# Kernel optimization log

Hardware: AMD Instinct MI355X
Metric: run time of the kernel (lower is better)

Reference implementation:

```python
import jax, jax.numpy as jnp
import numpy as np

EPS = 1e-5  # torch LayerNorm default

def ln(x, g, b):
    mu = jnp.mean(x, axis=-1, keepdims=True)
    var = jnp.mean((x - mu) ** 2, axis=-1, keepdims=True)
    return (x - mu) * jax.lax.rsqrt(var + EPS) * g + b

B, S, E, A = 131072, 199, 3, 32
D_IN = S + 1  # state_dim + 1 (time feature)

def setup_inputs() -> dict:
    key = jax.random.key(0)
    ks = iter(jax.random.split(key, 32))
    def w(shape, fan_in):
        lim = 1.0 / np.sqrt(fan_in)
        return jax.random.uniform(next(ks), shape, jnp.float32, -lim, lim)
    inp = {
        "state": jax.random.normal(next(ks), (B, S), jnp.float32),
        "time_delta": jax.random.uniform(next(ks), (B,), jnp.float32),
        # trunk: Linear(200,256)+LN, Linear(256,256)+LN, Linear(256,128)+LN
        "W1": w((D_IN, 256), D_IN), "b1": w((256,), D_IN),
        "g1": jnp.ones((256,), jnp.float32), "be1": jnp.zeros((256,), jnp.float32),
        "W2": w((256, 256), 256), "b2": w((256,), 256),
        "g2": jnp.ones((256,), jnp.float32), "be2": jnp.zeros((256,), jnp.float32),
        "W3": w((256, 128), 256), "b3": w((128,), 256),
        "g3": jnp.ones((128,), jnp.float32), "be3": jnp.zeros((128,), jnp.float32),
        # value stream
        "Wv1": w((128, 64), 128), "bv1": w((64,), 128),
        "gv": jnp.ones((64,), jnp.float32), "bev": jnp.zeros((64,), jnp.float32),
        "Wv2": w((64, 1), 64), "bv2": w((1,), 64),
        # E stacked advantage streams (all heads share action dim A)
        "Wa1": w((E, 128, 64), 128), "ba1": w((E, 64), 128),
        "ga": jnp.ones((E, 64), jnp.float32), "bea": jnp.zeros((E, 64), jnp.float32),
        "Wa2": w((E, 64, A), 64), "ba2": w((E, A), 64),
        "event_type": jax.random.randint(next(ks), (B,), 0, E),
    }
    return inp

def reference(state, time_delta,
              W1, b1, g1, be1, W2, b2, g2, be2, W3, b3, g3, be3,
              Wv1, bv1, gv, bev, Wv2, bv2,
              Wa1, ba1, ga, bea, Wa2, ba2, event_type):
    td = time_delta[:, None]                       # [B,1]
    x = jnp.concatenate([state, td], axis=1)       # [B,200]
    h = jax.nn.relu(ln(x @ W1 + b1, g1, be1))      # [B,256]
    h = jax.nn.relu(ln(h @ W2 + b2, g2, be2))      # [B,256]
    f = jax.nn.relu(ln(h @ W3 + b3, g3, be3))      # [B,128]
    v = jax.nn.relu(ln(f @ Wv1 + bv1, gv, bev)) @ Wv2 + bv2  # [B,1]
    # compute all E advantage heads, then per-sample select by event_type
    h1 = jnp.einsum('bd,edh->ebh', f, Wa1) + ba1[:, None, :]           # [E,B,64]
    h1 = jax.nn.relu(ln(h1, ga[:, None, :], bea[:, None, :]))
    adv_all = jnp.einsum('ebh,eha->eba', h1, Wa2) + ba2[:, None, :]    # [E,B,A]
    adv = jnp.take_along_axis(adv_all, event_type[None, :, None], axis=0)[0]  # [B,A]
    return v + (adv - adv.mean(axis=1, keepdims=True))
```

## Files before the change

kernel.cpp:

```cpp
#include <hip/hip_runtime.h>
#include <hip/hip_bf16.h>
#include <stdint.h>

#define DEV __device__ __forceinline__

typedef __attribute__((ext_vector_type(8))) short short8;
typedef __attribute__((ext_vector_type(4))) float floatx4;

constexpr int TM  = 64;
constexpr int NB  = 131072;
constexpr int AST = 264;

constexpr int OFF_W1 = 0;
constexpr int OFF_W2 = 57344;
constexpr int OFF_W3 = 122880;
constexpr int OFF_WH = 155648;
constexpr int OFF_WA2= 188416;
constexpr int NWQ    = 194560;

constexpr int C_B1=0, C_G1=256, C_BE1=512, C_B2=768, C_G2=1024, C_BE2=1280,
  C_B3=1536, C_G3=1664, C_BE3=1792, C_BV1=1920, C_GV=1984, C_BEV=2048,
  C_WV2=2112, C_BV2=2176, C_BA1=2180, C_GA=2372, C_BEA=2564, C_BA2=2756;
constexpr int NCONST=2852;

struct Ptrs {
  const float *state,*td,*W1,*b1,*g1,*be1,*W2,*b2,*g2,*be2,*W3,*b3,*g3,*be3,
    *Wv1,*bv1,*gv,*bev,*Wv2,*bv2,*Wa1,*ba1,*ga,*bea,*Wa2,*ba2;
  const int *et;
};

DEV unsigned short f2bf(float x){
  uint32_t u = __float_as_uint(x);
  u += 0x7fffu + ((u>>16)&1u);
  return (unsigned short)(u>>16);
}
DEV uint32_t f2bf_pk(float a, float b){
  float2 f2; f2.x=a; f2.y=b;
  __hip_bfloat162 h = __float22bfloat162_rn(f2);
  union { __hip_bfloat162 h; uint32_t u; } cv; cv.h = h;
  return cv.u;
}

__global__ void prep_kernel(Ptrs p, unsigned short* __restrict__ wq, float* __restrict__ cq){
  int idx = blockIdx.x*256 + threadIdx.x;
  if (idx < NWQ) {
    float v = 0.f;
    if (idx < OFF_W2) {
      int e = idx, w = e/14336, r = e%14336;
      int kc = r>>11, ct=(r>>9)&3, l=(r>>3)&63, j=r&7;
      int n = w*64 + ct*16 + (l&15);
      int k = kc*32 + (l>>4)*8 + j;
      if (k < 200) v = p.W1[k*256 + n];
      else if (k == 200) v = p.b1[n];
    } else if (idx < OFF_W3) {
      int e = idx-OFF_W2, w=e>>14, r=e&16383;
      int kc=r>>11, ct=(r>>9)&3, l=(r>>3)&63, j=r&7;
      int n = w*64 + ct*16 + (l&15);
      int k = kc*32 + (l>>4)*8 + j;
      v = p.W2[k*256 + n];
    } else if (idx < OFF_WH) {
      int e = idx-OFF_W3, w=e>>13, r=e&8191;
      int kc=r>>10, ct=(r>>9)&1, l=(r>>3)&63, j=r&7;
      int n = w*32 + ct*16 + (l&15);
      int k = kc*32 + (l>>4)*8 + j;
      v = p.W3[k*128 + n];
    } else if (idx < OFF_WA2) {
      int e = idx-OFF_WH, h=e>>13, r=e&8191;
      int kc=r>>11, ct=(r>>9)&3, l=(r>>3)&63, j=r&7;
      int n = ct*16 + (l&15);
      int k = kc*32 + (l>>4)*8 + j;
      v = (h<3) ? p.Wa1[h*8192 + k*64 + n] : p.Wv1[k*64 + n];
    } else {
      int e = idx-OFF_WA2, h=e>>11, r=e&2047;
      int kc=r>>10, ct=(r>>9)&1, l=(r>>3)&63, j=r&7;
      int n = ct*16 + (l&15);
      int k = kc*32 + (l>>4)*8 + j;
      v = p.Wa2[h*2048 + k*32 + n];
    }
    wq[idx] = f2bf(v);
  } else if (idx < NWQ + NCONST) {
    int ci = idx - NWQ;
    float v;
    if      (ci < 256)  v = p.b1[ci];
    else if (ci < 512)  v = p.g1[ci-256];
    else if (ci < 768)  v = p.be1[ci-512];
    else if (ci < 1024) v = p.b2[ci-768];
    else if (ci < 1280) v = p.g2[ci-1024];
    else if (ci < 1536) v = p.be2[ci-1280];
    else if (ci < 1664) v = p.b3[ci-1536];
    else if (ci < 1792) v = p.g3[ci-1664];
    else if (ci < 1920) v = p.be3[ci-1792];
    else if (ci < 1984) v = p.bv1[ci-1920];
    else if (ci < 2048) v = p.gv[ci-1984];
    else if (ci < 2112) v = p.bev[ci-2048];
    else if (ci < 2176) v = p.Wv2[ci-2112];
    else if (ci < 2180) v = (ci==2176) ? p.bv2[0] : 0.f;
    else if (ci < 2372) v = p.ba1[ci-2180];
    else if (ci < 2564) v = p.ga[ci-2372];
    else if (ci < 2756) v = p.bea[ci-2564];
    else                v = p.ba2[ci-2756];
    cq[ci] = v;
  }
}

template<int N>
DEV void loadB(short8 (&B)[N], const unsigned short* __restrict__ src, int lane){
  #pragma unroll
  for (int i=0;i<N;i++) B[i] = *(const short8*)(src + i*512 + lane*8);
}

template<int RT>
DEV void zeroAccT(floatx4 (&acc)[RT][4]){
  const floatx4 z = {0.f,0.f,0.f,0.f};
  #pragma unroll
  for (int rt=0;rt<RT;rt++)
    #pragma unroll
    for (int ct=0;ct<4;ct++) acc[rt][ct]=z;
}

template<int KC,int RT>
DEV void runGemmT(floatx4 (&acc)[RT][4], const short8 (&Bw)[KC*RT],
                  const unsigned short* aBase, int aOff){
  #pragma unroll
  for (int kc=0;kc<KC;kc++){
    short8 a[4];
    #pragma unroll
    for (int ct=0;ct<4;ct++)
      a[ct] = *(const short8*)(aBase + ct*16*AST + aOff + kc*32);
    #pragma unroll
    for (int rt=0;rt<RT;rt++)
      #pragma unroll
      for (int ct=0;ct<4;ct++)
        acc[rt][ct] = __builtin_amdgcn_mfma_f32_16x16x32_bf16(Bw[kc*RT+rt], a[ct], acc[rt][ct], 0,0,0);
  }
}

template<int RT,bool BIAS>
DEV void statsT(floatx4 (&acc)[RT][4], const float* __restrict__ cq, int bo,
                float* sbuf, float* ssbuf, int q, int ln){
  if constexpr (BIAS){
    #pragma unroll
    for (int rt=0;rt<RT;rt++){
      floatx4 b4 = *(const floatx4*)(cq + bo + rt*16 + q*4);
      #pragma unroll
      for (int ct=0;ct<4;ct++) acc[rt][ct] += b4;
    }
  }
  #pragma unroll
  for (int ct=0;ct<4;ct++){
    float s=0.f, ss=0.f;
    #pragma unroll
    for (int rt=0;rt<RT;rt++)
      #pragma unroll
      for (int r=0;r<4;r++){ float v=acc[rt][ct][r]; s+=v; ss+=v*v; }
    s += __shfl_xor(s,16); ss += __shfl_xor(ss,16);
    s += __shfl_xor(s,32); ss += __shfl_xor(ss,32);
    if (q==0){
      atomicAdd(&sbuf[ct*16+ln], s);
      atomicAdd(&ssbuf[ct*16+ln], ss);
    }
  }
}

template<int RT>
DEV void lnWriteT(const floatx4 (&acc)[RT][4], const float* __restrict__ cq, int go, int beo,
                  const float* sbuf, const float* ssbuf, float invN,
                  unsigned short* act_, int colBase, int q, int ln){
  float mu[4], rs[4];
  #pragma unroll
  for (int ct=0;ct<4;ct++){
    float sv = sbuf[ct*16+ln], ssv = ssbuf[ct*16+ln];
    mu[ct] = sv*invN;
    rs[ct] = rsqrtf(ssv*invN - mu[ct]*mu[ct] + 1e-5f);
  }
  #pragma unroll
  for (int rt=0;rt<RT;rt++){
    floatx4 g4  = *(const floatx4*)(cq + go  + rt*16 + q*4);
    floatx4 be4 = *(const floatx4*)(cq + beo + rt*16 + q*4);
    #pragma unroll
    for (int ct=0;ct<4;ct++){
      float y[4];
      #pragma unroll
      for (int r=0;r<4;r++)
        y[r] = fmaxf((acc[rt][ct][r]-mu[ct])*rs[ct]*g4[r]+be4[r], 0.f);
      uint2 pk; pk.x = f2bf_pk(y[0],y[1]); pk.y = f2bf_pk(y[2],y[3]);
      *(uint2*)(act_ + (ct*16+ln)*AST + colBase + rt*16 + q*4) = pk;
    }
  }
}

__global__ __launch_bounds__(256,4) void dqn_main(
    const float* __restrict__ state, const float* __restrict__ td,
    const int* __restrict__ et, const unsigned short* __restrict__ wq,
    const float* __restrict__ cq, float* __restrict__ out)
{
  __shared__ __align__(16) unsigned short act[TM*AST];
  __shared__ float sstat[2][2][64];
  __shared__ float vbuf[64];
  __shared__ int   etl[64];

  const int tid=threadIdx.x, w=tid>>6, lane=tid&63, q=lane>>4, ln=lane&15;
  const int rowBlk = blockIdx.x*TM;

  {
    ((float*)sstat)[tid] = 0.f;
    const float* sbase = state + (size_t)rowBlk*199;
    #pragma unroll
    for (int it=0; it<7; ++it){
      int t = tid + it*256;
      int r = t/28, c = t - r*28;
      unsigned short* dst = act + r*AST + c*8;
      if (c < 25){
        const float* src = sbase + r*199 + c*8;
        float v0=src[0], v1=src[1], v2=src[2], v3=src[3];
        float v4=src[4], v5=src[5], v6=src[6];
        int o7 = (c==24)? 198 : c*8+7;
        float s7 = sbase[r*199 + o7];
        float v7 = (c==24)? td[rowBlk+r] : s7;
        uint4 pk;
        pk.x=f2bf_pk(v0,v1); pk.y=f2bf_pk(v2,v3);
        pk.z=f2bf_pk(v4,v5); pk.w=f2bf_pk(v6,v7);
        *(uint4*)dst = pk;
      } else {
        uint4 pk{0u,0u,0u,0u};
        if (c==25) pk.x = 0x3F80u;
        *(uint4*)dst = pk;
      }
    }
    if (tid < 64) etl[tid] = et[rowBlk+tid];
  }
  __syncthreads();

  const unsigned short* aBase = act + ln*AST + q*8;
  floatx4 acc[4][4];

  {
    short8 Bw[28];
    loadB<28>(Bw, wq + OFF_W1 + w*14336, lane);
    zeroAccT<4>(acc);
    runGemmT<7,4>(acc, Bw, aBase, 0);
  }
  statsT<4,false>(acc, cq, 0, sstat[0][0], sstat[0][1], q, ln);
  __syncthreads();
  lnWriteT<4>(acc, cq, C_G1+w*64, C_BE1+w*64, sstat[0][0], sstat[0][1], 1.f/256.f, act, w*64, q, ln);
  __syncthreads();

  {
    short8 Bw[32];
    loadB<32>(Bw, wq + OFF_W2 + w*16384, lane);
    zeroAccT<4>(acc);
    runGemmT<8,4>(acc, Bw, aBase, 0);
  }
  statsT<4,true>(acc, cq, C_B2+w*64, sstat[1][0], sstat[1][1], q, ln);
  __syncthreads();
  if (tid < 128) ((float*)sstat[0])[tid] = 0.f;
  lnWriteT<4>(acc, cq, C_G2+w*64, C_BE2+w*64, sstat[1][0], sstat[1][1], 1.f/256.f, act, w*64, q, ln);
  __syncthreads();

  floatx4 acc3[2][4];
  {
    short8 Bw[16];
    loadB<16>(Bw, wq + OFF_W3 + w*8192, lane);
    zeroAccT<2>(acc3);
    runGemmT<8,2>(acc3, Bw, aBase, 0);
  }
  statsT<2,true>(acc3, cq, C_B3+w*32, sstat[0][0], sstat[0][1], q, ln);
  __syncthreads();
  lnWriteT<2>(acc3, cq, C_G3+w*32, C_BE3+w*32, sstat[0][0], sstat[0][1], 1.f/128.f, act, w*32, q, ln);
  __syncthreads();

  {
    short8 Bh[16];
    loadB<16>(Bh, wq + OFF_WH + w*8192, lane);
    zeroAccT<4>(acc);
    runGemmT<4,4>(acc, Bh, aBase, 0);
  }
  {
    const int bo = (w<3)? C_BA1+w*64 : C_BV1;
    const int go = (w<3)? C_GA +w*64 : C_GV;
    const int beo= (w<3)? C_BEA+w*64 : C_BEV;
    #pragma unroll
    for (int rt=0;rt<4;rt++){
      floatx4 b4 = *(const floatx4*)(cq + bo + rt*16 + q*4);
      #pragma unroll
      for (int ct=0;ct<4;ct++) acc[rt][ct] += b4;
    }
    float mu[4], rs[4];
    #pragma unroll
    for (int ct=0;ct<4;ct++){
      float s=0.f, ss=0.f;
      #pragma unroll
      for (int rt=0;rt<4;rt++)
        #pragma unroll
        for (int r=0;r<4;r++){ float v=acc[rt][ct][r]; s+=v; ss+=v*v; }
      s += __shfl_xor(s,16); ss += __shfl_xor(ss,16);
      s += __shfl_xor(s,32); ss += __shfl_xor(ss,32);
      mu[ct]=s*(1.f/64.f);
      rs[ct]=rsqrtf(ss*(1.f/64.f)-mu[ct]*mu[ct]+1e-5f);
    }
    #pragma unroll
    for (int rt=0;rt<4;rt++){
      floatx4 g4  = *(const floatx4*)(cq + go  + rt*16 + q*4);
      floatx4 be4 = *(const floatx4*)(cq + beo + rt*16 + q*4);
      #pragma unroll
      for (int ct=0;ct<4;ct++)
        #pragma unroll
        for (int r=0;r<4;r++)
          acc[rt][ct][r] = fmaxf((acc[rt][ct][r]-mu[ct])*rs[ct]*g4[r]+be4[r], 0.f);
    }
    if (w==3){
      float bv2v = cq[C_BV2];
      floatx4 wv4[4];
      #pragma unroll
      for (int rt=0;rt<4;rt++) wv4[rt] = *(const floatx4*)(cq + C_WV2 + rt*16 + q*4);
      #pragma unroll
      for (int ct=0;ct<4;ct++){
        float dot=0.f;
        #pragma unroll
        for (int rt=0;rt<4;rt++)
          #pragma unroll
          for (int r=0;r<4;r++) dot += acc[rt][ct][r]*wv4[rt][r];
        dot += __shfl_xor(dot,16);
        dot += __shfl_xor(dot,32);
        if (q==0) vbuf[ct*16+ln] = dot + bv2v;
      }
    }
  }
  __syncthreads();

  if (w<3){
    #pragma unroll
    for (int rt=0;rt<4;rt++)
      #pragma unroll
      for (int ct=0;ct<4;ct++){
        uint2 pk;
        pk.x = f2bf_pk(acc[rt][ct][0], acc[rt][ct][1]);
        pk.y = f2bf_pk(acc[rt][ct][2], acc[rt][ct][3]);
        *(uint2*)(act + (ct*16+ln)*AST + 64*w + rt*16 + q*4) = pk;
      }
    short8 B2[4];
    loadB<4>(B2, wq + OFF_WA2 + w*2048, lane);
    floatx4 acc2[2][4];
    zeroAccT<2>(acc2);
    runGemmT<2,2>(acc2, B2, aBase, 64*w);
    #pragma unroll
    for (int rt=0;rt<2;rt++){
      floatx4 b4 = *(const floatx4*)(cq + C_BA2 + w*32 + rt*16 + q*4);
      #pragma unroll
      for (int ct=0;ct<4;ct++) acc2[rt][ct] += b4;
    }
    #pragma unroll
    for (int ct=0;ct<4;ct++){
      float sm=0.f;
      #pragma unroll
      for (int rt=0;rt<2;rt++)
        #pragma unroll
        for (int r=0;r<4;r++) sm += acc2[rt][ct][r];
      sm += __shfl_xor(sm,16);
      sm += __shfl_xor(sm,32);
      int b = ct*16+ln;
      if (etl[b]==w){
        float vm = vbuf[b] - sm*(1.f/32.f);
        #pragma unroll
        for (int rt=0;rt<2;rt++){
          floatx4 o = acc2[rt][ct];
          o[0]+=vm; o[1]+=vm; o[2]+=vm; o[3]+=vm;
          *(floatx4*)(out + (size_t)(rowBlk+b)*32 + rt*16 + q*4) = o;
        }
      }
    }
  }
}

extern "C" void kernel_launch(void* const* d_in, const int* in_sizes, int n_in,
                              void* d_out, int out_size, void* d_ws, size_t ws_size,
                              hipStream_t stream)
{
  Ptrs p;
  p.state=(const float*)d_in[0];  p.td =(const float*)d_in[1];
  p.W1 =(const float*)d_in[2];  p.b1 =(const float*)d_in[3];  p.g1 =(const float*)d_in[4];  p.be1=(const float*)d_in[5];
  p.W2 =(const float*)d_in[6];  p.b2 =(const float*)d_in[7];  p.g2 =(const float*)d_in[8];  p.be2=(const float*)d_in[9];
  p.W3 =(const float*)d_in[10]; p.b3 =(const float*)d_in[11]; p.g3 =(const float*)d_in[12]; p.be3=(const float*)d_in[13];
  p.Wv1=(const float*)d_in[14]; p.bv1=(const float*)d_in[15]; p.gv =(const float*)d_in[16]; p.bev=(const float*)d_in[17];
  p.Wv2=(const float*)d_in[18]; p.bv2=(const float*)d_in[19];
  p.Wa1=(const float*)d_in[20]; p.ba1=(const float*)d_in[21]; p.ga =(const float*)d_in[22]; p.bea=(const float*)d_in[23];
  p.Wa2=(const float*)d_in[24]; p.ba2=(const float*)d_in[25];
  p.et =(const int*)d_in[26];

  unsigned short* wq = (unsigned short*)d_ws;
  float* cq = (float*)((char*)d_ws + (size_t)NWQ*2);

  const int prepN = NWQ + NCONST;
  hipLaunchKernelGGL(prep_kernel, dim3((prepN+255)/256), dim3(256), 0, stream, p, wq, cq);
  hipLaunchKernelGGL(dqn_main, dim3(NB/TM), dim3(256), 0, stream,
                     p.state, p.td, p.et, (const unsigned short*)wq, (const float*)cq, (float*)d_out);
}
```

Baseline: 284.8 us.

## Stream weight fragments per MFMA step and prefetch next layer's first tiles

Each GEMM no longer preloads its whole weight slice (up to 32 short8 registers) before computing. It now loads each B fragment from global memory right before its MFMA, and prefetches the first four fragments of the next layer during the previous layer's LayerNorm write, kept alive with an empty asm. LayerNorm statistics now go into per-wave LDS slots that are summed on read, replacing shared-memory atomics and the zeroing passes. The aim is lower register pressure, fewer atomics, and weight-load latency hidden behind barriers. The risk is global-load latency exposed inside the MFMA loop where the old bulk preload used to hide it.

```diff
diff --git a/kernel.cpp b/kernel.cpp
--- a/kernel.cpp
+++ b/kernel.cpp
@@ -40,6 +40,8 @@
   union { __hip_bfloat162 h; uint32_t u; } cv; cv.h = h;
   return cv.u;
 }
+
+DEV void keep8(const short8 &v){ asm volatile("" :: "v"(v)); }
 
 __global__ void prep_kernel(Ptrs p, unsigned short* __restrict__ wq, float* __restrict__ cq){
   int idx = blockIdx.x*256 + threadIdx.x;
@@ -103,12 +105,6 @@
   }
 }
 
-template<int N>
-DEV void loadB(short8 (&B)[N], const unsigned short* __restrict__ src, int lane){
-  #pragma unroll
-  for (int i=0;i<N;i++) B[i] = *(const short8*)(src + i*512 + lane*8);
-}
-
 template<int RT>
 DEV void zeroAccT(floatx4 (&acc)[RT][4]){
   const floatx4 z = {0.f,0.f,0.f,0.f};
@@ -119,25 +115,32 @@
 }
 
 template<int KC,int RT>
-DEV void runGemmT(floatx4 (&acc)[RT][4], const short8 (&Bw)[KC*RT],
-                  const unsigned short* aBase, int aOff){
+DEV void runGemmP(floatx4 (&acc)[RT][4], const unsigned short* __restrict__ wp,
+                  const unsigned short* __restrict__ aB, int aOff, int lane,
+                  const short8 (&pf)[4]){
   #pragma unroll
   for (int kc=0;kc<KC;kc++){
     short8 a[4];
     #pragma unroll
-    for (int ct=0;ct<4;ct++)
-      a[ct] = *(const short8*)(aBase + ct*16*AST + aOff + kc*32);
-    #pragma unroll
-    for (int rt=0;rt<RT;rt++)
-      #pragma unroll
-      for (int ct=0;ct<4;ct++)
-        acc[rt][ct] = __builtin_amdgcn_mfma_f32_16x16x32_bf16(Bw[kc*RT+rt], a[ct], acc[rt][ct], 0,0,0);
+    for (int c=0;c<4;c++)
+      a[c] = *(const short8*)(aB + c*16*AST + aOff + kc*32);
+    #pragma unroll
+    for (int rt=0;rt<RT;rt++){
+      short8 bw;
+      if constexpr (true){
+        if (kc*RT+rt < 4) bw = pf[kc*RT+rt];
+        else bw = *(const short8*)(wp + (kc*RT+rt)*512 + lane*8);
+      }
+      #pragma unroll
+      for (int c=0;c<4;c++)
+        acc[rt][c] = __builtin_amdgcn_mfma_f32_16x16x32_bf16(bw, a[c], acc[rt][c], 0,0,0);
+    }
   }
 }
 
 template<int RT,bool BIAS>
-DEV void statsT(floatx4 (&acc)[RT][4], const float* __restrict__ cq, int bo,
-                float* sbuf, float* ssbuf, int q, int ln){
+DEV void statsS(floatx4 (&acc)[RT][4], const float* __restrict__ cq, int bo,
+                float (&sst)[2][64][4], int w, int q, int ln){
   if constexpr (BIAS){
     #pragma unroll
     for (int rt=0;rt<RT;rt++){
@@ -156,22 +159,26 @@
     s += __shfl_xor(s,16); ss += __shfl_xor(ss,16);
     s += __shfl_xor(s,32); ss += __shfl_xor(ss,32);
     if (q==0){
-      atomicAdd(&sbuf[ct*16+ln], s);
-      atomicAdd(&ssbuf[ct*16+ln], ss);
+      sst[0][ct*16+ln][w] = s;
+      sst[1][ct*16+ln][w] = ss;
     }
   }
 }
 
 template<int RT>
-DEV void lnWriteT(const floatx4 (&acc)[RT][4], const float* __restrict__ cq, int go, int beo,
-                  const float* sbuf, const float* ssbuf, float invN,
+DEV void lnWriteS(const floatx4 (&acc)[RT][4], const float* __restrict__ cq, int go, int beo,
+                  const float (&sst)[2][64][4], float invN,
                   unsigned short* act_, int colBase, int q, int ln){
   float mu[4], rs[4];
   #pragma unroll
   for (int ct=0;ct<4;ct++){
-    float sv = sbuf[ct*16+ln], ssv = ssbuf[ct*16+ln];
+    int row = ct*16+ln;
+    floatx4 s4 = *(const floatx4*)&sst[0][row][0];
+    floatx4 q4 = *(const floatx4*)&sst[1][row][0];
+    float sv = (s4[0]+s4[1])+(s4[2]+s4[3]);
+    float qv = (q4[0]+q4[1])+(q4[2]+q4[3]);
     mu[ct] = sv*invN;
-    rs[ct] = rsqrtf(ssv*invN - mu[ct]*mu[ct] + 1e-5f);
+    rs[ct] = rsqrtf(qv*invN - mu[ct]*mu[ct] + 1e-5f);
   }
   #pragma unroll
   for (int rt=0;rt<RT;rt++){
@@ -195,15 +202,25 @@
     const float* __restrict__ cq, float* __restrict__ out)
 {
   __shared__ __align__(16) unsigned short act[TM*AST];
-  __shared__ float sstat[2][2][64];
+  __shared__ __align__(16) float sstat[2][64][4];
   __shared__ float vbuf[64];
   __shared__ int   etl[64];
 
   const int tid=threadIdx.x, w=tid>>6, lane=tid&63, q=lane>>4, ln=lane&15;
   const int rowBlk = blockIdx.x*TM;
 
+  const unsigned short* wl1 = wq + OFF_W1 + w*14336;
+  const unsigned short* wl2 = wq + OFF_W2 + w*16384;
+  const unsigned short* wl3 = wq + OFF_W3 + w*8192;
+  const unsigned short* wlh = wq + OFF_WH + w*8192;
+  const unsigned short* aBase = act + ln*AST + q*8;
+
+  short8 pf[4];
+
+  #pragma unroll
+  for (int i=0;i<4;i++) pf[i] = *(const short8*)(wl1 + i*512 + lane*8);
+
   {
-    ((float*)sstat)[tid] = 0.f;
     const float* sbase = state + (size_t)rowBlk*199;
     #pragma unroll
     for (int it=0; it<7; ++it){
@@ -229,52 +246,57 @@
     }
     if (tid < 64) etl[tid] = et[rowBlk+tid];
   }
-  __syncthreads();
-
-  const unsigned short* aBase = act + ln*AST + q*8;
+  #pragma unroll
+  for (int i=0;i<4;i++) keep8(pf[i]);
+  __syncthreads();
+
   floatx4 acc[4][4];
 
-  {
-    short8 Bw[28];
-    loadB<28>(Bw, wq + OFF_W1 + w*14336, lane);
-    zeroAccT<4>(acc);
-    runGemmT<7,4>(acc, Bw, aBase, 0);
-  }
-  statsT<4,false>(acc, cq, 0, sstat[0][0], sstat[0][1], q, ln);
-  __syncthreads();
-  lnWriteT<4>(acc, cq, C_G1+w*64, C_BE1+w*64, sstat[0][0], sstat[0][1], 1.f/256.f, act, w*64, q, ln);
-  __syncthreads();
-
-  {
-    short8 Bw[32];
-    loadB<32>(Bw, wq + OFF_W2 + w*16384, lane);
-    zeroAccT<4>(acc);
-    runGemmT<8,4>(acc, Bw, aBase, 0);
-  }
-  statsT<4,true>(acc, cq, C_B2+w*64, sstat[1][0], sstat[1][1], q, ln);
-  __syncthreads();
-  if (tid < 128) ((float*)sstat[0])[tid] = 0.f;
-  lnWriteT<4>(acc, cq, C_G2+w*64, C_BE2+w*64, sstat[1][0], sstat[1][1], 1.f/256.f, act, w*64, q, ln);
+  zeroAccT<4>(acc);
+  runGemmP<7,4>(acc, wl1, aBase, 0, lane, pf);
+  statsS<4,false>(acc, cq, 0, sstat, w, q, ln);
+  __syncthreads();
+
+  #pragma unroll
+  for (int i=0;i<4;i++) pf[i] = *(const short8*)(wl2 + i*512 + lane*8);
+  lnWriteS<4>(acc, cq, C_G1+w*64, C_BE1+w*64, sstat, 1.f/256.f, act, w*64, q, ln);
+  #pragma unroll
+  for (int i=0;i<4;i++) keep8(pf[i]);
+  __syncthreads();
+
+  zeroAccT<4>(acc);
+  runGemmP<8,4>(acc, wl2, aBase, 0, lane, pf);
+  statsS<4,true>(acc, cq, C_B2+w*64, sstat, w, q, ln);
+  __syncthreads();
+
+  #pragma unroll
+  for (int i=0;i<4;i++) pf[i] = *(const short8*)(wl3 + i*512 + lane*8);
+  lnWriteS<4>(acc, cq, C_G2+w*64, C_BE2+w*64, sstat, 1.f/256.f, act, w*64, q, ln);
+  #pragma unroll
+  for (int i=0;i<4;i++) keep8(pf[i]);
   __syncthreads();
 
   floatx4 acc3[2][4];
-  {
-    short8 Bw[16];
-    loadB<16>(Bw, wq + OFF_W3 + w*8192, lane);
-    zeroAccT<2>(acc3);
-    runGemmT<8,2>(acc3, Bw, aBase, 0);
-  }
-  statsT<2,true>(acc3, cq, C_B3+w*32, sstat[0][0], sstat[0][1], q, ln);
-  __syncthreads();
-  lnWriteT<2>(acc3, cq, C_G3+w*32, C_BE3+w*32, sstat[0][0], sstat[0][1], 1.f/128.f, act, w*32, q, ln);
-  __syncthreads();
-
-  {
-    short8 Bh[16];
-    loadB<16>(Bh, wq + OFF_WH + w*8192, lane);
-    zeroAccT<4>(acc);
-    runGemmT<4,4>(acc, Bh, aBase, 0);
-  }
+  zeroAccT<2>(acc3);
+  runGemmP<8,2>(acc3, wl3, aBase, 0, lane, pf);
+  statsS<2,true>(acc3, cq, C_B3+w*32, sstat, w, q, ln);
+  __syncthreads();
+
+  #pragma unroll
+  for (int i=0;i<4;i++) pf[i] = *(const short8*)(wlh + i*512 + lane*8);
+  lnWriteS<2>(acc3, cq, C_G3+w*32, C_BE3+w*32, sstat, 1.f/128.f, act, w*32, q, ln);
+  #pragma unroll
+  for (int i=0;i<4;i++) keep8(pf[i]);
+  __syncthreads();
+
+  short8 pfa[4];
+  if (w<3){
+    #pragma unroll
+    for (int i=0;i<4;i++)
+      pfa[i] = *(const short8*)(wq + OFF_WA2 + w*2048 + i*512 + lane*8);
+  }
+  zeroAccT<4>(acc);
+  runGemmP<4,4>(acc, wlh, aBase, 0, lane, pf);
   {
     const int bo = (w<3)? C_BA1+w*64 : C_BV1;
     const int go = (w<3)? C_GA +w*64 : C_GV;
@@ -326,6 +348,10 @@
       }
     }
   }
+  if (w<3){
+    #pragma unroll
+    for (int i=0;i<4;i++) keep8(pfa[i]);
+  }
   __syncthreads();
 
   if (w<3){
@@ -338,11 +364,20 @@
         pk.y = f2bf_pk(acc[rt][ct][2], acc[rt][ct][3]);
         *(uint2*)(act + (ct*16+ln)*AST + 64*w + rt*16 + q*4) = pk;
       }
-    short8 B2[4];
-    loadB<4>(B2, wq + OFF_WA2 + w*2048, lane);
     floatx4 acc2[2][4];
     zeroAccT<2>(acc2);
-    runGemmT<2,2>(acc2, B2, aBase, 64*w);
+    #pragma unroll
+    for (int kc=0;kc<2;kc++){
+      short8 a[4];
+      #pragma unroll
+      for (int c=0;c<4;c++)
+        a[c] = *(const short8*)(aBase + c*16*AST + 64*w + kc*32);
+      #pragma unroll
+      for (int rt=0;rt<2;rt++)
+        #pragma unroll
+        for (int c=0;c<4;c++)
+          acc2[rt][c] = __builtin_amdgcn_mfma_f32_16x16x32_bf16(pfa[kc*2+rt], a[c], acc2[rt][c], 0,0,0);
+    }
     #pragma unroll
     for (int rt=0;rt<2;rt++){
       floatx4 b4 = *(const floatx4*)(cq + C_BA2 + w*32 + rt*16 + q*4);
```

Measured after the change: 289.3 us. Within noise of the previous version (+1.6%).
